# Kernel optimization log

Hardware: AMD Instinct MI355X
Metric: run time of the kernel (lower is better)

The kernel has to match this reference:

```python
import jax, jax.numpy as jnp
import numpy as np

D_MODEL = 1024
NUM_NEURONS = 2048
BATCH = 64
LUT_SIZE = 4096


def setup_inputs() -> dict:
    key = jax.random.key(0)
    ks = jax.random.split(key, 6)
    x = jax.random.normal(ks[0], (BATCH, D_MODEL), dtype=jnp.float32)
    t = jax.random.uniform(ks[1], (BATCH,), dtype=jnp.float32)
    W = jax.random.normal(ks[2], (NUM_NEURONS, D_MODEL), dtype=jnp.float32) * 0.02
    B_p = jnp.zeros((NUM_NEURONS, D_MODEL), dtype=jnp.float32)
    # xavier_uniform with gain=0.5 for Linear(num_neurons -> d_model), weight shape (d_model, num_neurons)
    limit = 0.5 * np.sqrt(6.0 / (NUM_NEURONS + D_MODEL))
    proj_real_w = jax.random.uniform(ks[3], (D_MODEL, NUM_NEURONS), minval=-limit, maxval=limit, dtype=jnp.float32)
    proj_imag_w = jax.random.uniform(ks[4], (D_MODEL, NUM_NEURONS), minval=-limit, maxval=limit, dtype=jnp.float32)
    # sin/cos lookup tables over [0, 2pi)
    grid = jnp.arange(LUT_SIZE, dtype=jnp.float32) * (2.0 * np.pi / LUT_SIZE)
    sin_table = jnp.sin(grid)
    cos_table = jnp.cos(grid)
    return {"x": x, "t": t, "W": W, "B_p": B_p,
            "proj_real_w": proj_real_w, "proj_imag_w": proj_imag_w,
            "sin_table": sin_table, "cos_table": cos_table}


def _lut_sin_cos(theta, sin_table, cos_table):
    # LUT lookup with linear interpolation, period 2*pi
    L = sin_table.shape[0]
    pos = theta * (np.float32(L) / np.float32(2.0 * np.pi))
    base = jnp.floor(pos)
    frac = pos - base                      # in [0, 1)
    i0 = jnp.mod(base.astype(jnp.int32), L)
    i1 = jnp.mod(i0 + 1, L)
    s = sin_table[i0] * (1.0 - frac) + sin_table[i1] * frac
    c = cos_table[i0] * (1.0 - frac) + cos_table[i1] * frac
    return s, c


def reference(x, t, W, B_p, proj_real_w, proj_imag_w, sin_table, cos_table):
    # theta: (B, N, D)
    wavelength = 1.0 + jnp.abs(W)                       # (N, D)
    theta = x[:, None, :] / wavelength + B_p + t[:, None, None]
    sin_theta, cos_theta = _lut_sin_cos(theta, sin_table, cos_table)
    cos_sum = cos_theta.sum(axis=-1)                    # (B, N)
    sin_sum = sin_theta.sum(axis=-1)                    # (B, N)
    out = cos_sum @ proj_real_w.T + sin_sum @ proj_imag_w.T  # (B, D)
    return jax.nn.silu(out)
```

## Files before the change

kernel.cpp:

```cpp
#include <hip/hip_runtime.h>
#include <math.h>

#define INV2PI 0.15915494309189535f

__global__ __launch_bounds__(512) void k_sums(
    const float* __restrict__ x, const float* __restrict__ t,
    const float* __restrict__ W, const float* __restrict__ Bp,
    float2* __restrict__ S2)
{
    __shared__ float x_s[64 * 128];

    const int tid  = threadIdx.x;
    const int lane = tid & 63;
    const int wid  = __builtin_amdgcn_readfirstlane(tid >> 6);
    const int nl   = wid & 1;
    const int bq   = wid >> 1;
    const int n    = blockIdx.x * 2 + nl;

    float accC[16], accS[16];
    #pragma unroll
    for (int j = 0; j < 16; ++j) { accC[j] = 0.f; accS[j] = 0.f; }

    const float4* x4 = reinterpret_cast<const float4*>(x);

    for (int c = 0; c < 8; ++c) {
        __syncthreads();

        #pragma unroll
        for (int i = 0; i < 4; ++i) {
            int f4 = i * 512 + tid;
            int b  = f4 >> 5;
            int dq = f4 & 31;
            float4 v = x4[b * 256 + c * 32 + dq];
            *reinterpret_cast<float4*>(&x_s[f4 << 2]) = v;
        }

        float2 w2 = *reinterpret_cast<const float2*>(W  + (size_t)n * 1024 + c * 128 + 2 * lane);
        float2 b2 = *reinterpret_cast<const float2*>(Bp + (size_t)n * 1024 + c * 128 + 2 * lane);
        const float iwx = INV2PI / (1.f + fabsf(w2.x));
        const float iwy = INV2PI / (1.f + fabsf(w2.y));
        const float bpx = b2.x * INV2PI;
        const float bpy = b2.y * INV2PI;

        __syncthreads();

        #pragma unroll
        for (int j = 0; j < 16; ++j) {
            const float2 xv = *reinterpret_cast<const float2*>(
                &x_s[(bq * 16 + j) * 128 + 2 * lane]);
            float a, r;
            a = fmaf(xv.x, iwx, bpx); r = __builtin_amdgcn_fractf(a);
            accC[j] += __builtin_amdgcn_cosf(r);
            accS[j] += __builtin_amdgcn_sinf(r);
            a = fmaf(xv.y, iwy, bpy); r = __builtin_amdgcn_fractf(a);
            accC[j] += __builtin_amdgcn_cosf(r);
            accS[j] += __builtin_amdgcn_sinf(r);
        }
    }

    __syncthreads();
    float* sl = x_s + (wid << 10);
    const int g  = lane >> 4;
    const int bb = lane & 15;

    #pragma unroll
    for (int j = 0; j < 16; ++j) sl[j * 64 + (lane ^ j)] = accC[j];
    float sC = 0.f;
    #pragma unroll
    for (int k = 0; k < 16; ++k) sC += sl[bb * 64 + ((g * 16 + k) ^ bb)];

    #pragma unroll
    for (int j = 0; j < 16; ++j) sl[j * 64 + (lane ^ j)] = accS[j];
    float sS = 0.f;
    #pragma unroll
    for (int k = 0; k < 16; ++k) sS += sl[bb * 64 + ((g * 16 + k) ^ bb)];

    sC += __shfl_xor(sC, 16);
    sS += __shfl_xor(sS, 16);
    sC += __shfl_xor(sC, 32);
    sS += __shfl_xor(sS, 32);

    if (lane < 16) {
        const int b  = bq * 16 + lane;
        const float tv = t[b];
        const float ct = cosf(tv), st = sinf(tv);
        S2[n * 64 + b] = make_float2(ct * sC - st * sS,
                                     st * sC + ct * sS);
    }
}

__global__ __launch_bounds__(256) void k_gemm(
    const float2* __restrict__ S2, const float* __restrict__ Pr,
    const float* __restrict__ Pi, float* __restrict__ partial)
{
    const int lane = threadIdx.x & 63;
    const int wid  = __builtin_amdgcn_readfirstlane(threadIdx.x >> 6);
    const int d0   = blockIdx.x * 8 + wid * 2;
    const int k0   = blockIdx.y * 256;

    const float* pr = Pr + (size_t)d0 * 2048 + k0;
    const float* pi = Pi + (size_t)d0 * 2048 + k0;

    float a0 = 0.f, a1 = 0.f;

    for (int kk = 0; kk < 256; kk += 8) {
        float2 cs[8];
        #pragma unroll
        for (int i = 0; i < 8; ++i)
            cs[i] = S2[(size_t)(k0 + kk + i) * 64 + lane];
        #pragma unroll
        for (int i = 0; i < 8; ++i) {
            a0 += pr[kk + i]        * cs[i].x + pi[kk + i]        * cs[i].y;
            a1 += pr[2048 + kk + i] * cs[i].x + pi[2048 + kk + i] * cs[i].y;
        }
    }

    float* p = partial + ((size_t)blockIdx.y * 1024 + d0) * 64 + lane;
    p[0]  = a0;
    p[64] = a1;
}

__global__ __launch_bounds__(256, 4) void k_reduce_silu(
    const float* __restrict__ partial, float* __restrict__ out)
{
    const int lane = threadIdx.x & 63;
    const int gw   = blockIdx.x * 4 + (threadIdx.x >> 6);
    const int b    = gw >> 4;
    const int d    = ((gw & 15) << 6) + lane;

    float s = 0.f;
    #pragma unroll
    for (int ss = 0; ss < 8; ++ss)
        s += partial[((size_t)ss * 1024 + d) * 64 + b];

    float sig = 1.0f / (1.0f + __expf(-s));
    out[(size_t)b * 1024 + d] = s * sig;
}

extern "C" void kernel_launch(void* const* d_in, const int* in_sizes, int n_in,
                              void* d_out, int out_size, void* d_ws, size_t ws_size,
                              hipStream_t stream)
{
    const float* x  = (const float*)d_in[0];
    const float* t  = (const float*)d_in[1];
    const float* W  = (const float*)d_in[2];
    const float* Bp = (const float*)d_in[3];
    const float* Pr = (const float*)d_in[4];
    const float* Pi = (const float*)d_in[5];

    float*  out     = (float*)d_out;
    float2* S2      = (float2*)d_ws;
    float*  partial = (float*)((char*)d_ws + (1 << 20));

    k_sums<<<1024, 512, 0, stream>>>(x, t, W, Bp, S2);
    k_gemm<<<dim3(128, 8), 256, 0, stream>>>(S2, Pr, Pi, partial);
    k_reduce_silu<<<256, 256, 0, stream>>>(partial, out);
}
```

Before: 164.5 us.

## Drop LDS staging of x and compute two neurons per wave in k_sums

```diff
diff --git a/kernel.cpp b/kernel.cpp
--- a/kernel.cpp
+++ b/kernel.cpp
@@ -3,89 +3,116 @@
 
 #define INV2PI 0.15915494309189535f
 
-__global__ __launch_bounds__(512) void k_sums(
+
+__global__ __launch_bounds__(256) void k_sums(
     const float* __restrict__ x, const float* __restrict__ t,
     const float* __restrict__ W, const float* __restrict__ Bp,
     float2* __restrict__ S2)
 {
-    __shared__ float x_s[64 * 128];
+    __shared__ float sl_all[4][1024];
 
     const int tid  = threadIdx.x;
     const int lane = tid & 63;
-    const int wid  = __builtin_amdgcn_readfirstlane(tid >> 6);
-    const int nl   = wid & 1;
-    const int bq   = wid >> 1;
-    const int n    = blockIdx.x * 2 + nl;
+    const int w    = tid >> 6;
+    const int gw   = blockIdx.x * 4 + w;
+    const int n2   = gw >> 2;
+    const int bq   = gw & 3;
+    const int n0   = n2 * 2, n1 = n0 + 1;
 
-    float accC[16], accS[16];
+    float aC0[16], aS0[16], aC1[16], aS1[16];
     #pragma unroll
-    for (int j = 0; j < 16; ++j) { accC[j] = 0.f; accS[j] = 0.f; }
+    for (int j = 0; j < 16; ++j) { aC0[j]=0.f; aS0[j]=0.f; aC1[j]=0.f; aS1[j]=0.f; }
 
-    const float4* x4 = reinterpret_cast<const float4*>(x);
+    const float* xb = x + (size_t)(bq * 16) * 1024 + 2 * lane;
 
     for (int c = 0; c < 8; ++c) {
-        __syncthreads();
+        const int dof = c * 128;
+
+        const float2 w0 = *reinterpret_cast<const float2*>(W  + (size_t)n0 * 1024 + dof + 2 * lane);
+        const float2 w1 = *reinterpret_cast<const float2*>(W  + (size_t)n1 * 1024 + dof + 2 * lane);
+        const float2 p0 = *reinterpret_cast<const float2*>(Bp + (size_t)n0 * 1024 + dof + 2 * lane);
+        const float2 p1 = *reinterpret_cast<const float2*>(Bp + (size_t)n1 * 1024 + dof + 2 * lane);
+        const float iw0x = INV2PI / (1.f + fabsf(w0.x));
+        const float iw0y = INV2PI / (1.f + fabsf(w0.y));
+        const float iw1x = INV2PI / (1.f + fabsf(w1.x));
+        const float iw1y = INV2PI / (1.f + fabsf(w1.y));
+        const float bp0x = p0.x * INV2PI;
+        const float bp0y = p0.y * INV2PI;
+        const float bp1x = p1.x * INV2PI;
+        const float bp1y = p1.y * INV2PI;
 
         #pragma unroll
-        for (int i = 0; i < 4; ++i) {
-            int f4 = i * 512 + tid;
-            int b  = f4 >> 5;
-            int dq = f4 & 31;
-            float4 v = x4[b * 256 + c * 32 + dq];
-            *reinterpret_cast<float4*>(&x_s[f4 << 2]) = v;
-        }
+        for (int h = 0; h < 2; ++h) {
+            float2 xv[8];
+            #pragma unroll
+            for (int j = 0; j < 8; ++j)
+                xv[j] = *reinterpret_cast<const float2*>(xb + (size_t)(h * 8 + j) * 1024 + dof);
 
-        float2 w2 = *reinterpret_cast<const float2*>(W  + (size_t)n * 1024 + c * 128 + 2 * lane);
-        float2 b2 = *reinterpret_cast<const float2*>(Bp + (size_t)n * 1024 + c * 128 + 2 * lane);
-        const float iwx = INV2PI / (1.f + fabsf(w2.x));
-        const float iwy = INV2PI / (1.f + fabsf(w2.y));
-        const float bpx = b2.x * INV2PI;
-        const float bpy = b2.y * INV2PI;
-
-        __syncthreads();
-
-        #pragma unroll
-        for (int j = 0; j < 16; ++j) {
-            const float2 xv = *reinterpret_cast<const float2*>(
-                &x_s[(bq * 16 + j) * 128 + 2 * lane]);
-            float a, r;
-            a = fmaf(xv.x, iwx, bpx); r = __builtin_amdgcn_fractf(a);
-            accC[j] += __builtin_amdgcn_cosf(r);
-            accS[j] += __builtin_amdgcn_sinf(r);
-            a = fmaf(xv.y, iwy, bpy); r = __builtin_amdgcn_fractf(a);
-            accC[j] += __builtin_amdgcn_cosf(r);
-            accS[j] += __builtin_amdgcn_sinf(r);
+            #pragma unroll
+            for (int j = 0; j < 8; ++j) {
+                const int jj = h * 8 + j;
+                float r;
+                r = __builtin_amdgcn_fractf(fmaf(xv[j].x, iw0x, bp0x));
+                aC0[jj] += __builtin_amdgcn_cosf(r);
+                aS0[jj] += __builtin_amdgcn_sinf(r);
+                r = __builtin_amdgcn_fractf(fmaf(xv[j].y, iw0y, bp0y));
+                aC0[jj] += __builtin_amdgcn_cosf(r);
+                aS0[jj] += __builtin_amdgcn_sinf(r);
+                r = __builtin_amdgcn_fractf(fmaf(xv[j].x, iw1x, bp1x));
+                aC1[jj] += __builtin_amdgcn_cosf(r);
+                aS1[jj] += __builtin_amdgcn_sinf(r);
+                r = __builtin_amdgcn_fractf(fmaf(xv[j].y, iw1y, bp1y));
+                aC1[jj] += __builtin_amdgcn_cosf(r);
+                aS1[jj] += __builtin_amdgcn_sinf(r);
+            }
         }
     }
 
-    __syncthreads();
-    float* sl = x_s + (wid << 10);
+    float* sl = sl_all[w];
     const int g  = lane >> 4;
     const int bb = lane & 15;
 
-    #pragma unroll
-    for (int j = 0; j < 16; ++j) sl[j * 64 + (lane ^ j)] = accC[j];
-    float sC = 0.f;
-    #pragma unroll
-    for (int k = 0; k < 16; ++k) sC += sl[bb * 64 + ((g * 16 + k) ^ bb)];
+    float sC0, sS0, sC1, sS1;
+    {
+        #pragma unroll
+        for (int j = 0; j < 16; ++j) sl[j * 64 + (lane ^ j)] = aC0[j];
+        float s = 0.f;
+        #pragma unroll
+        for (int k = 0; k < 16; ++k) s += sl[bb * 64 + ((g * 16 + k) ^ bb)];
+        sC0 = s;
+        #pragma unroll
+        for (int j = 0; j < 16; ++j) sl[j * 64 + (lane ^ j)] = aS0[j];
+        s = 0.f;
+        #pragma unroll
+        for (int k = 0; k < 16; ++k) s += sl[bb * 64 + ((g * 16 + k) ^ bb)];
+        sS0 = s;
+        #pragma unroll
+        for (int j = 0; j < 16; ++j) sl[j * 64 + (lane ^ j)] = aC1[j];
+        s = 0.f;
+        #pragma unroll
+        for (int k = 0; k < 16; ++k) s += sl[bb * 64 + ((g * 16 + k) ^ bb)];
+        sC1 = s;
+        #pragma unroll
+        for (int j = 0; j < 16; ++j) sl[j * 64 + (lane ^ j)] = aS1[j];
+        s = 0.f;
+        #pragma unroll
+        for (int k = 0; k < 16; ++k) s += sl[bb * 64 + ((g * 16 + k) ^ bb)];
+        sS1 = s;
+    }
 
-    #pragma unroll
-    for (int j = 0; j < 16; ++j) sl[j * 64 + (lane ^ j)] = accS[j];
-    float sS = 0.f;
-    #pragma unroll
-    for (int k = 0; k < 16; ++k) sS += sl[bb * 64 + ((g * 16 + k) ^ bb)];
-
-    sC += __shfl_xor(sC, 16);
-    sS += __shfl_xor(sS, 16);
-    sC += __shfl_xor(sC, 32);
-    sS += __shfl_xor(sS, 32);
+    sC0 += __shfl_xor(sC0, 16);  sS0 += __shfl_xor(sS0, 16);
+    sC1 += __shfl_xor(sC1, 16);  sS1 += __shfl_xor(sS1, 16);
+    sC0 += __shfl_xor(sC0, 32);  sS0 += __shfl_xor(sS0, 32);
+    sC1 += __shfl_xor(sC1, 32);  sS1 += __shfl_xor(sS1, 32);
 
     if (lane < 16) {
         const int b  = bq * 16 + lane;
         const float tv = t[b];
         const float ct = cosf(tv), st = sinf(tv);
-        S2[n * 64 + b] = make_float2(ct * sC - st * sS,
-                                     st * sC + ct * sS);
+        S2[n0 * 64 + b] = make_float2(ct * sC0 - st * sS0,
+                                      st * sC0 + ct * sS0);
+        S2[n1 * 64 + b] = make_float2(ct * sC1 - st * sS1,
+                                      st * sC1 + ct * sS1);
     }
 }
 
@@ -152,7 +179,7 @@
     float2* S2      = (float2*)d_ws;
     float*  partial = (float*)((char*)d_ws + (1 << 20));
 
-    k_sums<<<1024, 512, 0, stream>>>(x, t, W, Bp, S2);
+    k_sums<<<1024, 256, 0, stream>>>(x, t, W, Bp, S2);
     k_gemm<<<dim3(128, 8), 256, 0, stream>>>(S2, Pr, Pi, partial);
     k_reduce_silu<<<256, 256, 0, stream>>>(partial, out);
 }
```

After: 154.6 us. 6.0% less time.
